# Performance work log

Measured on AMD Instinct MI355X. Metric: run time of the kernel, lower is better.

Reference implementation:

```python
import jax, jax.numpy as jnp
import numpy as np

BN_EPS = 1e-5

def _resample_map(n_out):
    # out[..., i::7, j::7] = crop[..., min(i,5)::6, min(j,5)::6]
    # => output position p maps to crop position 6*(p//7) + min(p%7, 5)
    p = np.arange(n_out)
    return jnp.asarray((p // 7) * 6 + np.minimum(p % 7, 5), dtype=jnp.int32)


def setup_inputs() -> dict:
    key = jax.random.key(0)
    k = jax.random.split(key, 6)
    B, C, H, W = 32, 512, 56, 56
    C2, Cout = 2 * C, 256
    x = jax.random.normal(k[0], (B, C, H, W), dtype=jnp.float32)
    bn_gamma = jax.random.uniform(k[1], (C2,), dtype=jnp.float32, minval=0.5, maxval=1.5)
    bn_beta = jax.random.normal(k[2], (C2,), dtype=jnp.float32) * 0.1
    bn_mean = jax.random.normal(k[3], (C2,), dtype=jnp.float32) * 0.1
    bn_var = jax.random.uniform(k[4], (C2,), dtype=jnp.float32, minval=0.5, maxval=1.5)
    conv_w = jax.random.normal(k[5], (Cout, C2), dtype=jnp.float32) * (1.0 / np.sqrt(C2))
    return {"x": x, "bn_gamma": bn_gamma, "bn_beta": bn_beta,
            "bn_mean": bn_mean, "bn_var": bn_var, "conv_w": conv_w}


def reference(x, bn_gamma, bn_beta, bn_mean, bn_var, conv_w):
    # checkerboard resample: crop 56->48, expand back 48 -> 56 via separable gather
    crop = x[:, :, 4:-4, 4:-4]                      # [B,C,48,48]
    idx = _resample_map(56)                         # [56]
    up = crop[:, :, idx, :][:, :, :, idx]           # [B,C,56,56]
    cat = jnp.concatenate([x, up], axis=1)          # [B,2C,56,56]
    # origin block: BN (inference) -> ReLU -> 1x1 conv -> AvgPool 2x2 s2
    inv = (bn_gamma / jnp.sqrt(bn_var + BN_EPS))[None, :, None, None]
    h = (cat - bn_mean[None, :, None, None]) * inv + bn_beta[None, :, None, None]
    h = jax.nn.relu(h)
    y = jnp.einsum('bchw,oc->bohw', h, conv_w)      # 1x1 conv, [B,256,56,56]
    b, o, H, W = y.shape
    y = y.reshape(b, o, H // 2, 2, W // 2, 2).mean(axis=(3, 5))  # [B,256,28,28]
    return y
```

## Files before the change

kernel.cpp:

```cpp
#include <hip/hip_runtime.h>

typedef float  floatx4 __attribute__((ext_vector_type(4)));
typedef float  float4a __attribute__((ext_vector_type(4), aligned(4)));
typedef short  short8  __attribute__((ext_vector_type(8)));
typedef short  short4v __attribute__((ext_vector_type(4)));
typedef int    intx4   __attribute__((ext_vector_type(4)));

#define NB   32
#define NC   512
#define NHW  3136

template<int N> struct IC { static constexpr int value = N; };

__device__ __forceinline__ int ridx(int p) {
    int q = p / 7;
    int r = p - q * 7;
    return q * 6 + (r < 5 ? r : 5);
}
__device__ __forceinline__ short f2bf(float f) {
    unsigned int x = __builtin_bit_cast(unsigned int, f);
    x += 0x7fffu + ((x >> 16) & 1u);
    return (short)(x >> 16);
}
__device__ __forceinline__ void gload_lds16(const void* g, void* l) {
    __builtin_amdgcn_global_load_lds(
        (const __attribute__((address_space(1))) unsigned int*)g,
        (__attribute__((address_space(3))) unsigned int*)l, 16, 0, 0);
}

__global__ __launch_bounds__(256)
void prep_kernel(const float* __restrict__ w,
                 const float* __restrict__ g_, const float* __restrict__ be_,
                 const float* __restrict__ mn_, const float* __restrict__ vr_,
                 short* __restrict__ wb, float* __restrict__ pbg)
{
    int id = (blockIdx.x * 256 + threadIdx.x) * 4;
    int c  = id & 1023;
    float4a v  = *(const float4a*)(w + id);
    float4a gg = *(const float4a*)(g_ + c);
    float4a vr = *(const float4a*)(vr_ + c);
    short4v s;
#pragma unroll
    for (int j = 0; j < 4; ++j) {
        float sc = gg[j] * rsqrtf(vr[j] + 1e-5f);
        s[j] = f2bf(v[j] * sc);
    }
    *(short4v*)(wb + id) = s;
    if (blockIdx.x == 0) {
        for (int cc2 = threadIdx.x; cc2 < 1024; cc2 += 256) {
            float sc = g_[cc2] * rsqrtf(vr_[cc2] + 1e-5f);
            pbg[cc2] = be_[cc2] / sc - mn_[cc2];
        }
    }
}

__global__ __launch_bounds__(256, 2)
void fused_bn_conv_pool(const float* __restrict__ x,
                        const float* __restrict__ pbg,
                        const short* __restrict__ wgt,
                        float* __restrict__ out)
{
    __shared__ char smem[65536];
    short* WtB[2] = { (short*)(smem),         (short*)(smem + 32768) };
    short* AtB[2] = { (short*)(smem + 16384), (short*)(smem + 49152) };
    float* ys = (float*)smem;

    const int t    = threadIdx.x;
    const int bx0  = blockIdx.x;
    const int bx   = (bx0 & 7) * 224 + (bx0 >> 3);
    const int site = bx >> 1;
    const int nt   = bx & 1;
    const int b    = site / 28;
    const int ph   = site - b * 28;

    const int cc     = t & 7;
    const int mg     = t >> 3;
    const int m_base = mg * 4;
    const bool realm = (m_base < 112);
    const int rr = (m_base >= 56) ? 1 : 0;
    const int w0 = m_base - rr * 56;
    const int hs = 4 + ridx(2 * ph + rr);
    const int c0 = ridx(w0);
    const int offg = hs * 56 + 4 + c0;
    int d_[4];
#pragma unroll
    for (int j = 0; j < 4; ++j) d_[j] = ridx(w0 + j) - c0;
    const int xb   = b * NC * NHW;
    const int offd = 112 * ph + m_base;

    const int lid = t & 63;
    const int wv  = t >> 6;
    const int wo  = wv & 1;
    const int wm  = wv >> 1;
    const int col = lid & 15;
    const int q4  = lid >> 4;
    const int obw = wo * 64;
    const int mbw = wm * 64;
    const int sw  = col & 7;

    floatx4 acc[4][4];
#pragma unroll
    for (int i = 0; i < 4; ++i)
#pragma unroll
        for (int j = 0; j < 4; ++j)
            acc[i][j] = (floatx4){0.f, 0.f, 0.f, 0.f};

    const short* wrow = wgt + nt * 128 * 1024;

    float4a pf[2][8];

    auto load_into = [&](int kc, auto ic) {
        constexpr int S = decltype(ic)::value;
        if (!realm) return;
        const int k0 = kc * 64;
        const int cb = k0 + cc * 8;
        if (k0 < 512) {
#pragma unroll
            for (int i = 0; i < 8; ++i)
                pf[S][i] = *(const float4a*)(x + xb + (cb + i) * NHW + offd);
        } else {
#pragma unroll
            for (int i = 0; i < 8; ++i)
                pf[S][i] = *(const float4a*)(x + xb + (cb + i - 512) * NHW + offg);
        }
    };

    auto body = [&](int kc, short* Wt, short* At, auto ic) {
        constexpr int S = decltype(ic)::value;
        const int k0 = kc * 64;
        const int cb = k0 + cc * 8;
#pragma unroll
        for (int it = 0; it < 4; ++it) {
            int q = it * 256 + t;
            int o = q >> 3, sl = q & 7;
            gload_lds16(wrow + o * 1024 + k0 + ((sl ^ (o & 7)) * 8), Wt + q * 8);
        }
        {
            const bool upper = (k0 >= 512);
            intx4 vj[4];
#pragma unroll
            for (int j = 0; j < 4; ++j) vj[j] = (intx4){0, 0, 0, 0};
            if (realm) {
                float4a tLo = *(const float4a*)(pbg + cb);
                float4a tHi = *(const float4a*)(pbg + cb + 4);
                float rprev[4];
#pragma unroll
                for (int i = 0; i < 8; ++i) {
                    const float tch = (i < 4) ? tLo[i] : tHi[i - 4];
                    float vv[4];
                    if (!upper) {
#pragma unroll
                        for (int j = 0; j < 4; ++j) vv[j] = pf[S][i][j];
                    } else {
#pragma unroll
                        for (int j = 0; j < 4; ++j) {
                            int dd = d_[j];
                            float a  = (dd >= 2) ? pf[S][i][2] : pf[S][i][0];
                            float bq = (dd >= 2) ? pf[S][i][3] : pf[S][i][1];
                            vv[j] = (dd & 1) ? bq : a;
                        }
                    }
                    if (!(i & 1)) {
#pragma unroll
                        for (int j = 0; j < 4; ++j) rprev[j] = fmaxf(vv[j] + tch, 0.f);
                    } else {
#pragma unroll
                        for (int j = 0; j < 4; ++j) {
                            float rc = fmaxf(vv[j] + tch, 0.f);
                            unsigned pk;
                            asm("v_cvt_pk_bf16_f32 %0, %1, %2"
                                : "=v"(pk) : "v"(rprev[j]), "v"(rc));
                            vj[j][i >> 1] = (int)pk;
                        }
                    }
                }
            }
#pragma unroll
            for (int j = 0; j < 4; ++j) {
                int m = m_base + j;
                *(intx4*)(At + m * 64 + ((cc ^ (m & 7)) * 8)) = vj[j];
            }
        }
        __syncthreads();

        if (kc < 14) load_into(kc + 2, ic);

#pragma unroll
        for (int ks = 0; ks < 2; ++ks) {
            const int cb2 = ks * 4 + q4;
            short8 af[4], bf[4];
#pragma unroll
            for (int of = 0; of < 4; ++of) {
                int row = obw + of * 16 + col;
                af[of] = *(const short8*)(Wt + row * 64 + ((cb2 ^ sw) * 8));
            }
#pragma unroll
            for (int mf = 0; mf < 4; ++mf) {
                int row = mbw + mf * 16 + col;
                bf[mf] = *(const short8*)(At + row * 64 + ((cb2 ^ sw) * 8));
            }
#pragma unroll
            for (int of = 0; of < 4; ++of)
#pragma unroll
                for (int mf = 0; mf < 4; ++mf)
                    acc[of][mf] = __builtin_amdgcn_mfma_f32_16x16x32_bf16(
                        af[of], bf[mf], acc[of][mf], 0, 0, 0);
        }
    };

    load_into(0, IC<0>{});
    load_into(1, IC<1>{});

    for (int kc2 = 0; kc2 < 16; kc2 += 2) {
        body(kc2,     WtB[0], AtB[0], IC<0>{});
        body(kc2 + 1, WtB[1], AtB[1], IC<1>{});
    }

    __syncthreads();

#pragma unroll
    for (int s = 0; s < 4; ++s) {
        if (wo == (s >> 1)) {
#pragma unroll
            for (int of2 = 0; of2 < 2; ++of2) {
                const int of  = (s & 1) * 2 + of2;
                const int olb = of2 * 16 + q4 * 4;
#pragma unroll
                for (int mf = 0; mf < 4; ++mf) {
                    const int m = mbw + mf * 16 + col;
#pragma unroll
                    for (int rg = 0; rg < 4; ++rg)
                        ys[(olb + rg) * 132 + m] = acc[of][mf][rg];
                }
            }
        }
        __syncthreads();
        for (int i = t; i < 896; i += 256) {
            int ol = i / 28;
            int pw = i - ol * 28;
            const float* yr = ys + ol * 132 + 2 * pw;
            float v = (yr[0] + yr[1] + yr[56] + yr[57]) * 0.25f;
            int og = nt * 128 + s * 32 + ol;
            out[((b * 256 + og) * 28 + ph) * 28 + pw] = v;
        }
        __syncthreads();
    }
}

extern "C" void kernel_launch(void* const* d_in, const int* in_sizes, int n_in,
                              void* d_out, int out_size, void* d_ws, size_t ws_size,
                              hipStream_t stream) {
    (void)in_sizes; (void)n_in; (void)out_size; (void)ws_size;
    const float* x  = (const float*)d_in[0];
    const float* g  = (const float*)d_in[1];
    const float* be = (const float*)d_in[2];
    const float* mn = (const float*)d_in[3];
    const float* vr = (const float*)d_in[4];
    const float* w  = (const float*)d_in[5];
    float* o   = (float*)d_out;
    short* wb  = (short*)d_ws;
    float* pbg = (float*)((char*)d_ws + 524288);

    prep_kernel<<<dim3(256), dim3(256), 0, stream>>>(w, g, be, mn, vr, wb, pbg);
    fused_bn_conv_pool<<<dim3(32 * 28 * 2), dim3(256), 0, stream>>>(x, pbg, wb, o);
}
```

Before: 427.6 us.

## Prefetch next weight tile during MFMA with manual waitcnt and barrier

Measured after the change: 430.3 us. No clear change (+0.6%).

```diff
diff --git a/kernel.cpp b/kernel.cpp
--- a/kernel.cpp
+++ b/kernel.cpp
@@ -61,6 +61,7 @@
                         float* __restrict__ out)
 {
     __shared__ char smem[65536];
+    __shared__ float pbgs[1024];
     short* WtB[2] = { (short*)(smem),         (short*)(smem + 32768) };
     short* AtB[2] = { (short*)(smem + 16384), (short*)(smem + 49152) };
     float* ys = (float*)smem;
@@ -107,6 +108,9 @@
 
     const short* wrow = wgt + nt * 128 * 1024;
 
+    *(float4a*)(pbgs + t * 4) = *(const float4a*)(pbg + t * 4);
+    __syncthreads();
+
     float4a pf[2][8];
 
     auto load_into = [&](int kc, auto ic) {
@@ -125,24 +129,30 @@
         }
     };
 
-    auto body = [&](int kc, short* Wt, short* At, auto ic) {
-        constexpr int S = decltype(ic)::value;
-        const int k0 = kc * 64;
-        const int cb = k0 + cc * 8;
+    auto issue_wt = [&](int kcn, short* WtDst) {
+        const int k0n = kcn * 64;
 #pragma unroll
         for (int it = 0; it < 4; ++it) {
             int q = it * 256 + t;
             int o = q >> 3, sl = q & 7;
-            gload_lds16(wrow + o * 1024 + k0 + ((sl ^ (o & 7)) * 8), Wt + q * 8);
-        }
+            gload_lds16(wrow + o * 1024 + k0n + ((sl ^ (o & 7)) * 8), WtDst + q * 8);
+        }
+    };
+
+    auto body = [&](int kc, short* Wt, short* WtNext, short* At, auto ic, auto lastc) {
+        constexpr int S    = decltype(ic)::value;
+        constexpr int LAST = decltype(lastc)::value;
+        const int k0 = kc * 64;
+        const int cb = k0 + cc * 8;
+
         {
             const bool upper = (k0 >= 512);
             intx4 vj[4];
 #pragma unroll
             for (int j = 0; j < 4; ++j) vj[j] = (intx4){0, 0, 0, 0};
             if (realm) {
-                float4a tLo = *(const float4a*)(pbg + cb);
-                float4a tHi = *(const float4a*)(pbg + cb + 4);
+                float4a tLo = *(const float4a*)(pbgs + cb);
+                float4a tHi = *(const float4a*)(pbgs + cb + 4);
                 float rprev[4];
 #pragma unroll
                 for (int i = 0; i < 8; ++i) {
@@ -181,10 +191,19 @@
                 *(intx4*)(At + m * 64 + ((cc ^ (m & 7)) * 8)) = vj[j];
             }
         }
-        __syncthreads();
-
+
+        if (LAST) { asm volatile("s_waitcnt vmcnt(0)" ::: "memory"); }
+        else      { asm volatile("s_waitcnt vmcnt(8)" ::: "memory"); }
+        asm volatile("s_waitcnt lgkmcnt(0)" ::: "memory");
+        __builtin_amdgcn_sched_barrier(0);
+        __builtin_amdgcn_s_barrier();
+        __builtin_amdgcn_sched_barrier(0);
+
+        if (kc < 15) issue_wt(kc + 1, WtNext);
+        __builtin_amdgcn_sched_barrier(0);
         if (kc < 14) load_into(kc + 2, ic);
 
+        __builtin_amdgcn_s_setprio(1);
 #pragma unroll
         for (int ks = 0; ks < 2; ++ks) {
             const int cb2 = ks * 4 + q4;
@@ -206,15 +225,20 @@
                     acc[of][mf] = __builtin_amdgcn_mfma_f32_16x16x32_bf16(
                         af[of], bf[mf], acc[of][mf], 0, 0, 0);
         }
+        __builtin_amdgcn_s_setprio(0);
     };
 
+    issue_wt(0, WtB[0]);
+    __builtin_amdgcn_sched_barrier(0);
     load_into(0, IC<0>{});
     load_into(1, IC<1>{});
 
-    for (int kc2 = 0; kc2 < 16; kc2 += 2) {
-        body(kc2,     WtB[0], AtB[0], IC<0>{});
-        body(kc2 + 1, WtB[1], AtB[1], IC<1>{});
-    }
+    for (int kc2 = 0; kc2 < 14; kc2 += 2) {
+        body(kc2,     WtB[0], WtB[1], AtB[0], IC<0>{}, IC<0>{});
+        body(kc2 + 1, WtB[1], WtB[0], AtB[1], IC<1>{}, IC<0>{});
+    }
+    body(14, WtB[0], WtB[1], AtB[0], IC<0>{}, IC<0>{});
+    body(15, WtB[1], WtB[0], AtB[1], IC<1>{}, IC<1>{});
 
     __syncthreads();
 
```
